# Kernel tuning notes

Hardware: AMD Instinct MI355X
Metric: run time of the kernel (lower is better)

## Reference

```python
import jax, jax.numpy as jnp
import numpy as np

N_MET = 250_000
N_RXN = 500_000
E_SUB = 2_000_000
E_ALL = 4_000_000
HIDDEN = 64
MSG_DIM = 32
DT = 0.01  # flux-limiting step size (forward called with dt > 0)


def setup_inputs() -> dict:
    key = jax.random.key(0)
    ks = jax.random.split(key, 12)
    inp = {}
    inp["x"] = jax.random.uniform(ks[0], (N_MET, 8), dtype=jnp.float32)
    inp["met_sub"] = jax.random.randint(ks[1], (E_SUB,), 0, N_MET, dtype=jnp.int32)
    inp["rxn_sub"] = jax.random.randint(ks[2], (E_SUB,), 0, N_RXN, dtype=jnp.int32)
    inp["sto_sub"] = jax.random.uniform(ks[3], (E_SUB,), dtype=jnp.float32) + 0.5  # |s_ij| > 0
    inp["met_all"] = jax.random.randint(ks[4], (E_ALL,), 0, N_MET, dtype=jnp.int32)
    inp["rxn_all"] = jax.random.randint(ks[5], (E_ALL,), 0, N_RXN, dtype=jnp.int32)
    inp["sto_all"] = jax.random.normal(ks[6], (E_ALL,), dtype=jnp.float32)
    sc = lambda fan_in: 1.0 / np.sqrt(fan_in)
    inp["W1"] = jax.random.normal(ks[7], (2, HIDDEN), dtype=jnp.float32) * sc(2)
    inp["b1"] = jnp.zeros((HIDDEN,), jnp.float32)
    inp["W2"] = jax.random.normal(ks[8], (HIDDEN, MSG_DIM), dtype=jnp.float32) * sc(HIDDEN)
    inp["b2"] = jnp.zeros((MSG_DIM,), jnp.float32)
    inp["W3"] = jax.random.normal(ks[9], (MSG_DIM, HIDDEN), dtype=jnp.float32) * sc(MSG_DIM)
    inp["b3"] = jnp.zeros((HIDDEN,), jnp.float32)
    inp["W4"] = jax.random.normal(ks[10], (HIDDEN, 1), dtype=jnp.float32) * sc(HIDDEN)
    inp["b4"] = jnp.zeros((1,), jnp.float32)
    inp["log_k"] = jax.random.uniform(ks[11], (N_RXN,), dtype=jnp.float32, minval=-3.0, maxval=-1.0)
    return inp


def reference(x, met_sub, rxn_sub, sto_sub, met_all, rxn_all, sto_all,
              W1, b1, W2, b2, W3, b3, W4, b4, log_k):
    conc = x[:, 3]                                            # [n_met]
    # per-substrate-edge message: MLP([conc_src, |s|]) -> msg_dim
    msg_in = jnp.stack([conc[met_sub], sto_sub], axis=-1)     # [E_sub, 2]
    msg = jnp.tanh(msg_in @ W1 + b1) @ W2 + b2                # [E_sub, msg_dim]
    # aggregate messages per reaction (index_add)
    h_rxn = jax.ops.segment_sum(msg, rxn_sub, num_segments=N_RXN)  # [n_rxn, msg_dim]
    # non-negative rates
    k = jnp.power(10.0, log_k)
    r = (jnp.tanh(h_rxn @ W3 + b3) @ W4 + b4)[:, 0]           # [n_rxn]
    v = k * jax.nn.softplus(r)
    # flux limiting: scale rates so no substrate is over-consumed in one dt step
    consumption = sto_sub * v[rxn_sub] * DT                   # [E_sub]
    total = jax.ops.segment_sum(consumption, met_sub, num_segments=N_MET)
    active = total > 1e-12
    met_scale = jnp.where(active,
                          jnp.minimum(conc / jnp.where(active, total, 1.0), 1.0),
                          1.0)                                # [n_met]
    edge_scale = met_scale[met_sub]
    rxn_scale = jnp.ones((N_RXN,), v.dtype).at[rxn_sub].min(edge_scale)  # amin, include_self
    v = v * rxn_scale
    # dx/dt = scatter-add of signed stoich * rate over all edges
    contrib = sto_all * v[rxn_all]                            # [E_all]
    dxdt = jax.ops.segment_sum(contrib, met_all, num_segments=N_MET)
    return dxdt[:, None]                                      # [n_met, 1]
```

## Files before the change

### kernel.cpp

```cpp
#include <hip/hip_runtime.h>

#define N_MET 250000
#define N_RXN 500000
#define N_RXN_PAD 500032
#define E_SUB 2000000
#define E_ALL 4000000
#define DT 0.01f

#define RXN_PER_BLK 256
#define THREADS 256
#define EDGE_CAP 1536

#define MV_RPB 64

#define BINSZ 1024
#define NBINS ((N_MET + BINSZ - 1) / BINSZ)
#define PART_EPB 4096
#define PART_NBLK ((E_ALL + PART_EPB - 1) / PART_EPB)
#define SPART_NBLK ((E_SUB + PART_EPB - 1) / PART_EPB)
#define RBINSZ 1024
#define RNBINS ((N_RXN + RBINSZ - 1) / RBINSZ)
#define RPART_NBLK ((E_SUB + PART_EPB - 1) / PART_EPB)
#define RBIN_CAP 6144

typedef int v4i __attribute__((ext_vector_type(4)));
typedef float v4f __attribute__((ext_vector_type(4)));
typedef short bf16x8 __attribute__((ext_vector_type(8)));
typedef float f32x4 __attribute__((ext_vector_type(4)));

static __device__ __forceinline__ float fast_tanh(float x) {
  float e = __expf(x + x);
  return 1.0f - __fdividef(2.0f, e + 1.0f);
}

static __device__ __forceinline__ int bcast_i(int v, int lane) {
  return __builtin_amdgcn_readlane(v, lane);
}

static __device__ __forceinline__ unsigned short bf16_rn(float f) {
  unsigned u = __float_as_uint(f);
  unsigned r = u + 0x7FFFu + ((u >> 16) & 1u);
  return (unsigned short)(r >> 16);
}

__global__ void k_pre(const float* __restrict__ W2, const float* __restrict__ W3,
                      const float* __restrict__ b2,
                      uint4* __restrict__ wfh, uint4* __restrict__ wfl,
                      float* __restrict__ b2w3) {
  int tid = blockIdx.x * blockDim.x + threadIdx.x;
  if (tid < 512) {
    int lane = tid & 63, jt = (tid >> 6) & 3, ks = tid >> 8;
    int jj = jt * 16 + (lane & 15);
    unsigned short h[8], l[8];
    #pragma unroll
    for (int t = 0; t < 8; ++t) {
      int kk = ks * 32 + (lane >> 4) * 8 + t;
      float w = 0.f;
      #pragma unroll
      for (int m = 0; m < 32; ++m) w = fmaf(W2[kk * 32 + m], W3[m * 64 + jj], w);
      h[t] = bf16_rn(w);
      float hf = __uint_as_float(((unsigned)h[t]) << 16);
      l[t] = bf16_rn(w - hf);
    }
    uint4 H, L;
    H.x = (unsigned)h[0] | ((unsigned)h[1] << 16);
    H.y = (unsigned)h[2] | ((unsigned)h[3] << 16);
    H.z = (unsigned)h[4] | ((unsigned)h[5] << 16);
    H.w = (unsigned)h[6] | ((unsigned)h[7] << 16);
    L.x = (unsigned)l[0] | ((unsigned)l[1] << 16);
    L.y = (unsigned)l[2] | ((unsigned)l[3] << 16);
    L.z = (unsigned)l[4] | ((unsigned)l[5] << 16);
    L.w = (unsigned)l[6] | ((unsigned)l[7] << 16);
    int idx = (ks * 4 + jt) * 64 + lane;
    wfh[idx] = H; wfl[idx] = L;
  }
  if (tid < 64) {
    float t = 0.f;
    #pragma unroll
    for (int m = 0; m < 32; ++m) t = fmaf(b2[m], W3[m * 64 + tid], t);
    b2w3[tid] = t;
  }
}

__global__ void k_conc(const float* __restrict__ x, float* __restrict__ conc) {
  int m = blockIdx.x * blockDim.x + threadIdx.x;
  if (m < N_MET) conc[m] = __builtin_nontemporal_load(x + m * 8 + 3);
}


template <int NB>
static __device__ __forceinline__ void bc_body(const int* __restrict__ keys, int nkeys,
                                               int* __restrict__ blk_cnt, int nblk) {
  __shared__ int cnt[NB];
  int b = blockIdx.x, t = threadIdx.x;
  for (int i = t; i < NB; i += 256) cnt[i] = 0;
  __syncthreads();
  int base = b * PART_EPB;
  #pragma unroll
  for (int i = 0; i < PART_EPB / 256; ++i) {
    int e = base + i * 256 + t;
    if (e < nkeys) atomicAdd(&cnt[__builtin_nontemporal_load(keys + e) >> 10], 1);
  }
  __syncthreads();
  for (int i = t; i < NB; i += 256) blk_cnt[i * nblk + b] = cnt[i];
}

__global__ __launch_bounds__(256) void k_bc_all(const int* __restrict__ met_all,
                                                int* __restrict__ blk_cnt) {
  bc_body<NBINS>(met_all, E_ALL, blk_cnt, PART_NBLK);
}
__global__ __launch_bounds__(256) void k_bc_sub(const int* __restrict__ met_sub,
                                                int* __restrict__ blk_cnt) {
  bc_body<NBINS>(met_sub, E_SUB, blk_cnt, SPART_NBLK);
}
__global__ __launch_bounds__(256) void k_rbc(const int* __restrict__ rxn_sub,
                                             int* __restrict__ blk_cnt) {
  bc_body<RNBINS>(rxn_sub, E_SUB, blk_cnt, RPART_NBLK);
}

__global__ __launch_bounds__(256) void k_bscan1(const int* __restrict__ blk_cnt,
                                                int* __restrict__ blk_pref,
                                                int* __restrict__ bin_tot, int nblk) {
  __shared__ int ss[256];
  int j = blockIdx.x, t = threadIdx.x;
  int carry = 0;
  for (int c = 0; c < nblk; c += 256) {
    int idx = c + t;
    int v = (idx < nblk) ? blk_cnt[j * nblk + idx] : 0;
    ss[t] = v; __syncthreads();
    for (int d = 1; d < 256; d <<= 1) {
      int a = (t >= d) ? ss[t - d] : 0;
      __syncthreads();
      ss[t] += a;
      __syncthreads();
    }
    if (idx < nblk) blk_pref[j * nblk + idx] = carry + ss[t] - v;
    carry += ss[255];
    __syncthreads();
  }
  if (t == 0) bin_tot[j] = carry;
}

__global__ __launch_bounds__(512) void k_bscan2(const int* __restrict__ bin_tot,
                                                int* __restrict__ bin_start, int n) {
  __shared__ int ss[512];
  int t = threadIdx.x;
  int v = (t < n) ? bin_tot[t] : 0;
  ss[t] = v; __syncthreads();
  for (int d = 1; d < 512; d <<= 1) {
    int a = (t >= d) ? ss[t - d] : 0;
    __syncthreads();
    ss[t] += a;
    __syncthreads();
  }
  if (t < n) bin_start[t] = ss[t] - v;
}

template <int NB, typename MakeRec>
static __device__ __forceinline__ void part_sorted(
    const int* __restrict__ keys, int nkeys, int nblk,
    const int* __restrict__ blk_pref, const int* __restrict__ bin_start,
    int2* __restrict__ out, MakeRec make) {
  __shared__ int2 ordered[PART_EPB];
  __shared__ unsigned short binb[PART_EPB];
  __shared__ int cnt[NB];
  __shared__ int gofs[NB];
  __shared__ int ss[256];
  int b = blockIdx.x, t = threadIdx.x;
  for (int i = t; i < NB; i += 256) cnt[i] = 0;
  __syncthreads();
  int base = b * PART_EPB;
  int kbuf[PART_EPB / 256];
  #pragma unroll
  for (int i = 0; i < PART_EPB / 256; ++i) {
    int e = base + i * 256 + t;
    kbuf[i] = (e < nkeys) ? __builtin_nontemporal_load(keys + e) : -1;
    if (kbuf[i] >= 0) atomicAdd(&cnt[kbuf[i] >> 10], 1);
  }
  __syncthreads();
  int nloc = 0;
  for (int c = 0; c < NB; c += 256) {
    int idx = c + t;
    int v = (idx < NB) ? cnt[idx] : 0;
    ss[t] = v; __syncthreads();
    for (int d = 1; d < 256; d <<= 1) {
      int a = (t >= d) ? ss[t - d] : 0;
      __syncthreads();
      ss[t] += a;
      __syncthreads();
    }
    int tot = ss[255];
    if (idx < NB) {
      int ls = nloc + ss[t] - v;
      cnt[idx] = ls;
      gofs[idx] = bin_start[idx] + blk_pref[idx * nblk + b] - ls;
    }
    nloc += tot;
    __syncthreads();
  }
  #pragma unroll
  for (int i = 0; i < PART_EPB / 256; ++i) {
    int k = kbuf[i];
    if (k >= 0) {
      int e = base + i * 256 + t;
      int bin = k >> 10;
      int2 rec = make(e, k);
      int pos = atomicAdd(&cnt[bin], 1);
      ordered[pos] = rec;
      binb[pos] = (unsigned short)bin;
    }
  }
  __syncthreads();
  for (int i = t; i < nloc; i += 256) {
    int2 rec = ordered[i];
    out[gofs[binb[i]] + i] = rec;
  }
}

__global__ __launch_bounds__(256) void k_rpart(
    const int* __restrict__ rxn_sub, const int* __restrict__ met_sub,
    const float* __restrict__ sto_sub,
    const int* __restrict__ blk_pref, const int* __restrict__ bin_start,
    int2* __restrict__ bins_rxn) {
  part_sorted<RNBINS>(rxn_sub, E_SUB, RPART_NBLK, blk_pref, bin_start, bins_rxn,
    [=] __device__ (int e, int k) {
      int m = __builtin_nontemporal_load(met_sub + e);
      float st = __builtin_nontemporal_load(sto_sub + e);
      int2 rec; rec.x = ((k & (RBINSZ - 1)) << 18) | m; rec.y = __float_as_int(st);
      return rec;
    });
}

__global__ __launch_bounds__(256) void k_part_sub(
    const int* __restrict__ met_sub, const int* __restrict__ rxn_sub,
    const float* __restrict__ sto_sub, const float* __restrict__ v_pre,
    const int* __restrict__ blk_pref, const int* __restrict__ bin_start,
    int2* __restrict__ bins_sub) {
  part_sorted<NBINS>(met_sub, E_SUB, SPART_NBLK, blk_pref, bin_start, bins_sub,
    [=] __device__ (int e, int k) {
      int r = __builtin_nontemporal_load(rxn_sub + e);
      float st = __builtin_nontemporal_load(sto_sub + e);
      float val = st * v_pre[r] * DT;
      int2 rec; rec.x = k & (BINSZ - 1); rec.y = __float_as_int(val);
      return rec;
    });
}

__global__ __launch_bounds__(256) void k_part(
    const int* __restrict__ met_all, const int* __restrict__ rxn_all,
    const float* __restrict__ sto_all, const float* __restrict__ vfin,
    const int* __restrict__ blk_pref, const int* __restrict__ bin_start,
    int2* __restrict__ bins) {
  part_sorted<NBINS>(met_all, E_ALL, PART_NBLK, blk_pref, bin_start, bins,
    [=] __device__ (int e, int k) {
      int r = __builtin_nontemporal_load(rxn_all + e);
      float st = __builtin_nontemporal_load(sto_all + e);
      float val = st * vfin[r];
      int2 rec; rec.x = k & (BINSZ - 1); rec.y = __float_as_int(val);
      return rec;
    });
}

__global__ __launch_bounds__(256) void k_rbin(
    const int2* __restrict__ bins_rxn, const int* __restrict__ rbin_start,
    const int* __restrict__ rbin_tot, int2* __restrict__ edges8, int* __restrict__ off) {
  __shared__ int2 stage[RBIN_CAP];
  __shared__ int lcnt[RBINSZ];
  __shared__ int lcur[RBINSZ];
  __shared__ int ss[256];
  int j = blockIdx.x, t = threadIdx.x;
  int base = rbin_start[j], n = rbin_tot[j];
  for (int i = t; i < RBINSZ; i += 256) lcnt[i] = 0;
  __syncthreads();
  bool fits = (n <= RBIN_CAP);
  if (fits) {
    for (int i = t; i < n; i += 256) {
      int2 rec = bins_rxn[base + i];
      stage[i] = rec;
      atomicAdd(&lcnt[((unsigned)rec.x) >> 18], 1);
    }
  } else {
    for (int i = t; i < n; i += 256) {
      int2 rec = bins_rxn[base + i];
      atomicAdd(&lcnt[((unsigned)rec.x) >> 18], 1);
    }
  }
  __syncthreads();
  int s0 = lcnt[4 * t], s1 = lcnt[4 * t + 1], s2 = lcnt[4 * t + 2], s3 = lcnt[4 * t + 3];
  int tsum = s0 + s1 + s2 + s3;
  ss[t] = tsum; __syncthreads();
  for (int d = 1; d < 256; d <<= 1) {
    int a = (t >= d) ? ss[t - d] : 0;
    __syncthreads();
    ss[t] += a;
    __syncthreads();
  }
  int run = ss[t] - tsum;
  lcur[4 * t] = run;
  lcur[4 * t + 1] = run + s0;
  lcur[4 * t + 2] = run + s0 + s1;
  lcur[4 * t + 3] = run + s0 + s1 + s2;
  __syncthreads();
  int R0 = j * RBINSZ;
  for (int rl = t; rl < RBINSZ; rl += 256) {
    int r = R0 + rl;
    if (r < N_RXN) off[r] = base + lcur[rl];
  }
  if (j == 0 && t == 0) off[N_RXN] = E_SUB;
  __syncthreads();
  if (fits) {
    for (int i = t; i < n; i += 256) {
      int2 rec = stage[i];
      int pos = atomicAdd(&lcur[((unsigned)rec.x) >> 18], 1);
      int2 out; out.x = rec.x & 0x3FFFF; out.y = rec.y;
      edges8[base + pos] = out;
    }
  } else {
    for (int i = t; i < n; i += 256) {
      int2 rec = bins_rxn[base + i];
      int pos = atomicAdd(&lcur[((unsigned)rec.x) >> 18], 1);
      int2 out; out.x = rec.x & 0x3FFFF; out.y = rec.y;
      edges8[base + pos] = out;
    }
  }
}

static __device__ __forceinline__ float edge_sum_lds(int o0, int o1, int estart,
                                                     const float2* ep,
                                                     float w1x, float w1y, float b1j) {
  float T0 = 0.f, T1 = 0.f;
  int c = o0;
  for (; c + 1 < o1; c += 2) {
    float2 e0 = ep[c - estart];
    float2 e1 = ep[c + 1 - estart];
    T0 += fast_tanh(fmaf(e0.x, w1x, fmaf(e0.y, w1y, b1j)));
    T1 += fast_tanh(fmaf(e1.x, w1x, fmaf(e1.y, w1y, b1j)));
  }
  if (c < o1) {
    float2 e0 = ep[c - estart];
    T0 += fast_tanh(fmaf(e0.x, w1x, fmaf(e0.y, w1y, b1j)));
  }
  return T0 + T1;
}

static __device__ __forceinline__ float edge_sum_glob(int o0, int o1,
                                                      const int2* edges8,
                                                      const float* conc,
                                                      float w1x, float w1y, float b1j) {
  float T = 0.f;
  for (int c = o0; c < o1; ++c) {
    int2 rec = edges8[c];
    float cc = conc[rec.x];
    T += fast_tanh(fmaf(cc, w1x, fmaf(__int_as_float(rec.y), w1y, b1j)));
  }
  return T;
}

__global__ __launch_bounds__(THREADS) void k_edge(
    const int* __restrict__ off, const int2* __restrict__ edges8,
    const float* __restrict__ conc,
    const float* __restrict__ W1, const float* __restrict__ b1,
    unsigned short* __restrict__ Thi, unsigned short* __restrict__ Tlo, int use_lo) {
  __shared__ int off_s[RXN_PER_BLK + 1];
  __shared__ float2 se[EDGE_CAP];

  int tid = threadIdx.x;
  int lane = tid & 63;
  int wv = tid >> 6;
  int R0 = blockIdx.x * RXN_PER_BLK;

  for (int i = tid; i <= RXN_PER_BLK; i += THREADS) {
    int r = R0 + i;
    off_s[i] = off[r > N_RXN ? N_RXN : r];
  }
  __syncthreads();
  int estart = off_s[0];
  int nE = off_s[RXN_PER_BLK] - estart;
  bool fits = (nE <= EDGE_CAP);
  if (fits) {
    for (int i = tid; i < nE; i += THREADS) {
      int2 rec = edges8[estart + i];
      se[i] = make_float2(conc[rec.x], __int_as_float(rec.y));
    }
  }

  float w1x = W1[lane], w1y = W1[64 + lane], b1j = b1[lane];

  int rbase = R0 + wv * 64;
  int o0l = off_s[wv * 64 + lane];
  int o1l = off_s[wv * 64 + lane + 1];

  __syncthreads();

  #pragma clang loop unroll(disable)
  for (int i = 0; i < 64; ++i) {
    int r = rbase + i;
    if (r >= N_RXN) break;
    int o0 = bcast_i(o0l, i), o1 = bcast_i(o1l, i);
    float T = fits ? edge_sum_lds(o0, o1, estart, se, w1x, w1y, b1j)
                   : edge_sum_glob(o0, o1, edges8, conc, w1x, w1y, b1j);
    unsigned short hi = bf16_rn(T);
    Thi[r * 64 + lane] = hi;
    if (use_lo) {
      float hf = __uint_as_float(((unsigned)hi) << 16);
      Tlo[r * 64 + lane] = bf16_rn(T - hf);
    }
  }
}

__global__ __launch_bounds__(256) void k_mv(
    const int* __restrict__ off,
    const unsigned short* __restrict__ Thi, const unsigned short* __restrict__ Tlo,
    const uint4* __restrict__ wfh, const uint4* __restrict__ wfl,
    const float* __restrict__ b2w3, const float* __restrict__ b3,
    const float* __restrict__ W4, const float* __restrict__ b4,
    const float* __restrict__ log_k, int use_lo, float* __restrict__ v_pre) {
  __shared__ int soff[MV_RPB + 1];
  int tid = threadIdx.x, lane = tid & 63, w = tid >> 6;
  int B0 = blockIdx.x * MV_RPB;
  for (int i = tid; i <= MV_RPB; i += 256) {
    int r = B0 + i;
    soff[i] = off[r > N_RXN ? N_RXN : r];
  }
  __syncthreads();

  int R0 = B0 + w * 16;
  int col = lane & 15, rowg = lane >> 4;

  bf16x8 ah[2], al[2];
  {
    int rowelem = (R0 + col) * 64 + rowg * 8;
    const uint4* ph = (const uint4*)Thi;
    ah[0] = __builtin_bit_cast(bf16x8, ph[rowelem >> 3]);
    ah[1] = __builtin_bit_cast(bf16x8, ph[(rowelem + 32) >> 3]);
    if (use_lo) {
      const uint4* pl = (const uint4*)Tlo;
      al[0] = __builtin_bit_cast(bf16x8, pl[rowelem >> 3]);
      al[1] = __builtin_bit_cast(bf16x8, pl[(rowelem + 32) >> 3]);
    }
  }

  f32x4 acc[4];
  #pragma unroll
  for (int jt = 0; jt < 4; ++jt) acc[jt] = (f32x4){0.f, 0.f, 0.f, 0.f};

  #pragma unroll
  for (int jt = 0; jt < 4; ++jt) {
    #pragma unroll
    for (int ks = 0; ks < 2; ++ks) {
      int bidx = (ks * 4 + jt) * 64 + lane;
      bf16x8 bh = __builtin_bit_cast(bf16x8, wfh[bidx]);
      acc[jt] = __builtin_amdgcn_mfma_f32_16x16x32_bf16(ah[ks], bh, acc[jt], 0, 0, 0);
      if (use_lo) {
        bf16x8 bl = __builtin_bit_cast(bf16x8, wfl[bidx]);
        acc[jt] = __builtin_amdgcn_mfma_f32_16x16x32_bf16(ah[ks], bl, acc[jt], 0, 0, 0);
        acc[jt] = __builtin_amdgcn_mfma_f32_16x16x32_bf16(al[ks], bh, acc[jt], 0, 0, 0);
      }
    }
  }

  float w4c[4], bwc[4], b3c[4];
  #pragma unroll
  for (int jt = 0; jt < 4; ++jt) {
    int jj = jt * 16 + col;
    w4c[jt] = W4[jj]; bwc[jt] = b2w3[jj]; b3c[jt] = b3[jj];
  }
  float b40 = b4[0];

  float nq[4];
  #pragma unroll
  for (int q = 0; q < 4; ++q) {
    int idx = w * 16 + rowg * 4 + q;
    nq[q] = (float)(soff[idx + 1] - soff[idx]);
  }

  #pragma unroll
  for (int q = 0; q < 4; ++q) {
    float s = 0.f;
    #pragma unroll
    for (int jt = 0; jt < 4; ++jt) {
      float u = acc[jt][q] + nq[q] * bwc[jt] + b3c[jt];
      s += fast_tanh(u) * w4c[jt];
    }
    s += __shfl_xor(s, 1, 64);
    s += __shfl_xor(s, 2, 64);
    s += __shfl_xor(s, 4, 64);
    s += __shfl_xor(s, 8, 64);
    if (col == 0) {
      int r = R0 + rowg * 4 + q;
      float lk = (r < N_RXN) ? log_k[r] : 0.f;
      float racc = s + b40;
      float k10 = __expf(lk * 2.3025850929940457f);
      float sp = (racc > 15.f) ? racc : __logf(1.f + __expf(racc));
      if (r < N_RXN) v_pre[r] = k10 * sp;
    }
  }
}

__global__ __launch_bounds__(256) void k_bins_sub(
    const int2* __restrict__ bins_sub, const int* __restrict__ bin_start,
    const int* __restrict__ bin_tot, const float* __restrict__ conc,
    float* __restrict__ met_scale) {
  __shared__ float acc[BINSZ];
  int j = blockIdx.x, t = threadIdx.x;
  for (int i = t; i < BINSZ; i += 256) acc[i] = 0.f;
  __syncthreads();
  int s0 = bin_start[j], n = bin_tot[j];
  for (int i = t; i < n; i += 256) {
    int2 rec = bins_sub[s0 + i];
    atomicAdd(&acc[rec.x], __int_as_float(rec.y));
  }
  __syncthreads();
  int m0 = j * BINSZ;
  for (int i = t; i < BINSZ; i += 256) {
    int m = m0 + i;
    if (m < N_MET) {
      float tot = acc[i];
      met_scale[m] = (tot > 1e-12f) ? fminf(conc[m] / tot, 1.0f) : 1.0f;
    }
  }
}

__global__ __launch_bounds__(256) void k_rscale(
    const int* __restrict__ off, const int2* __restrict__ edges8,
    const float* __restrict__ met_scale, const float* __restrict__ v_pre,
    float* __restrict__ vfin) {
  __shared__ int soff[MV_RPB + 1];
  int tid = threadIdx.x, lane = tid & 63, w = tid >> 6;
  int B0 = blockIdx.x * MV_RPB;
  for (int i = tid; i <= MV_RPB; i += 256) {
    int r = B0 + i;
    soff[i] = off[r > N_RXN ? N_RXN : r];
  }
  __syncthreads();

  int rloc = w * 16 + (lane >> 2);
  int o0 = soff[rloc], o1 = soff[rloc + 1];
  float sc = 1.0f;
  for (int c = o0 + (lane & 3); c < o1; c += 4) {
    sc = fminf(sc, met_scale[edges8[c].x]);
  }
  sc = fminf(sc, __shfl_xor(sc, 1, 64));
  sc = fminf(sc, __shfl_xor(sc, 2, 64));
  if ((lane & 3) == 0) {
    int r = B0 + rloc;
    if (r < N_RXN) vfin[r] = v_pre[r] * sc;
  }
}

__global__ __launch_bounds__(256) void k_bins(const int2* __restrict__ bins,
                                              const int* __restrict__ bin_start,
                                              const int* __restrict__ bin_tot,
                                              float* __restrict__ dxdt) {
  __shared__ float acc[BINSZ];
  int j = blockIdx.x, t = threadIdx.x;
  for (int i = t; i < BINSZ; i += 256) acc[i] = 0.f;
  __syncthreads();
  int s0 = bin_start[j], n = bin_tot[j];
  for (int i = t; i < n; i += 256) {
    int2 rec = bins[s0 + i];
    atomicAdd(&acc[rec.x], __int_as_float(rec.y));
  }
  __syncthreads();
  int m0 = j * BINSZ;
  for (int i = t; i < BINSZ; i += 256) {
    int m = m0 + i;
    if (m < N_MET) dxdt[m] = acc[i];
  }
}

extern "C" void kernel_launch(void* const* d_in, const int* in_sizes, int n_in,
                              void* d_out, int out_size, void* d_ws, size_t ws_size,
                              hipStream_t stream) {
  const float* x       = (const float*)d_in[0];
  const int*   met_sub = (const int*)d_in[1];
  const int*   rxn_sub = (const int*)d_in[2];
  const float* sto_sub = (const float*)d_in[3];
  const int*   met_all = (const int*)d_in[4];
  const int*   rxn_all = (const int*)d_in[5];
  const float* sto_all = (const float*)d_in[6];
  const float* W1    = (const float*)d_in[7];
  const float* b1    = (const float*)d_in[8];
  const float* W2    = (const float*)d_in[9];
  const float* b2    = (const float*)d_in[10];
  const float* W3    = (const float*)d_in[11];
  const float* b3    = (const float*)d_in[12];
  const float* W4    = (const float*)d_in[13];
  const float* b4    = (const float*)d_in[14];
  const float* log_k = (const float*)d_in[15];
  float* dxdt = (float*)d_out;

  char* ws = (char*)d_ws;
  size_t p = 0;
  auto alloc = [&](size_t bytes) -> void* {
    void* r = (void*)(ws + p);
    p += (bytes + 255) & ~(size_t)255;
    return r;
  };
  int*    off        = (int*)alloc(sizeof(int) * (N_RXN + 1));
  uint4*  wfh        = (uint4*)alloc(sizeof(uint4) * 512);
  uint4*  wfl        = (uint4*)alloc(sizeof(uint4) * 512);
  float*  b2w3       = (float*)alloc(sizeof(float) * 64);
  float*  v_pre      = (float*)alloc(sizeof(float) * N_RXN);
  float*  vfin       = (float*)alloc(sizeof(float) * N_RXN);
  float*  conc       = (float*)alloc(sizeof(float) * N_MET);
  float*  met_scale  = (float*)alloc(sizeof(float) * N_MET);
  int2*   edges8     = (int2*)alloc(sizeof(int2) * E_SUB);
  int2*   bins_rxn   = (int2*)alloc(sizeof(int2) * E_SUB);
  int2*   bins_sub   = (int2*)alloc(sizeof(int2) * E_SUB);
  int2*   bins       = (int2*)alloc(sizeof(int2) * E_ALL);
  int*    rblk_cnt   = (int*)alloc(sizeof(int) * RNBINS * RPART_NBLK);
  int*    rblk_pref  = (int*)alloc(sizeof(int) * RNBINS * RPART_NBLK);
  int*    sblk_cnt   = (int*)alloc(sizeof(int) * NBINS * SPART_NBLK);
  int*    sblk_pref  = (int*)alloc(sizeof(int) * NBINS * SPART_NBLK);
  int*    blk_cnt    = (int*)alloc(sizeof(int) * NBINS * PART_NBLK);
  int*    blk_pref   = (int*)alloc(sizeof(int) * NBINS * PART_NBLK);
  int*    rbin_tot   = (int*)alloc(sizeof(int) * 512);
  int*    rbin_start = (int*)alloc(sizeof(int) * 512);
  int*    sbin_tot   = (int*)alloc(sizeof(int) * 512);
  int*    sbin_start = (int*)alloc(sizeof(int) * 512);
  int*    bin_tot    = (int*)alloc(sizeof(int) * 512);
  int*    bin_start  = (int*)alloc(sizeof(int) * 512);
  unsigned short* Thi = (unsigned short*)alloc(sizeof(unsigned short) * (size_t)N_RXN_PAD * 64);
  size_t tlo_bytes = sizeof(unsigned short) * (size_t)N_RXN_PAD * 64;
  int use_lo = (p + tlo_bytes <= ws_size) ? 1 : 0;
  unsigned short* Tlo = use_lo ? (unsigned short*)alloc(tlo_bytes) : Thi;
  (void)in_sizes; (void)n_in; (void)out_size;


  k_pre<<<2, 256, 0, stream>>>(W2, W3, b2, wfh, wfl, b2w3);
  k_conc<<<(N_MET + 255) / 256, 256, 0, stream>>>(x, conc);

  k_rbc<<<RPART_NBLK, 256, 0, stream>>>(rxn_sub, rblk_cnt);
  k_bc_sub<<<SPART_NBLK, 256, 0, stream>>>(met_sub, sblk_cnt);
  k_bc_all<<<PART_NBLK, 256, 0, stream>>>(met_all, blk_cnt);
  k_bscan1<<<RNBINS, 256, 0, stream>>>(rblk_cnt, rblk_pref, rbin_tot, RPART_NBLK);
  k_bscan1<<<NBINS, 256, 0, stream>>>(sblk_cnt, sblk_pref, sbin_tot, SPART_NBLK);
  k_bscan1<<<NBINS, 256, 0, stream>>>(blk_cnt, blk_pref, bin_tot, PART_NBLK);
  k_bscan2<<<1, 512, 0, stream>>>(rbin_tot, rbin_start, RNBINS);
  k_bscan2<<<1, 512, 0, stream>>>(sbin_tot, sbin_start, NBINS);
  k_bscan2<<<1, 512, 0, stream>>>(bin_tot, bin_start, NBINS);

  k_rpart<<<RPART_NBLK, 256, 0, stream>>>(rxn_sub, met_sub, sto_sub,
                                          rblk_pref, rbin_start, bins_rxn);
  k_rbin<<<RNBINS, 256, 0, stream>>>(bins_rxn, rbin_start, rbin_tot, edges8, off);

  k_edge<<<(N_RXN + RXN_PER_BLK - 1) / RXN_PER_BLK, THREADS, 0, stream>>>(
      off, edges8, conc, W1, b1, Thi, Tlo, use_lo);
  k_mv<<<(N_RXN + MV_RPB - 1) / MV_RPB, 256, 0, stream>>>(
      off, Thi, Tlo, wfh, wfl, b2w3, b3, W4, b4, log_k, use_lo, v_pre);

  k_part_sub<<<SPART_NBLK, 256, 0, stream>>>(met_sub, rxn_sub, sto_sub, v_pre,
                                             sblk_pref, sbin_start, bins_sub);
  k_bins_sub<<<NBINS, 256, 0, stream>>>(bins_sub, sbin_start, sbin_tot, conc, met_scale);

  k_rscale<<<(N_RXN + MV_RPB - 1) / MV_RPB, 256, 0, stream>>>(
      off, edges8, met_scale, v_pre, vfin);

  k_part<<<PART_NBLK, 256, 0, stream>>>(met_all, rxn_all, sto_all, vfin,
                                        blk_pref, bin_start, bins);
  k_bins<<<NBINS, 256, 0, stream>>>(bins, bin_start, bin_tot, dxdt);
}
```

Before: 516.7 us.

## Merge preprocessing launches and simplify per-edge tanh accumulation

Eleven small setup launches (weight precompute, conc extraction, three bin-count passes, and three pairs of scans) become three kernels that pick their role from the block index, cutting launch overhead and serial gaps. The per-edge tanh sum is rewritten as count minus twice a sum of 1/(exp2(k*t)+1), with the 2*log2(e) constant folded into W1 and b1, so each edge costs one exp2 and one reciprocal. The loop also carries o0 forward instead of reading it per reaction. This trades slight numerical differences from the hardware rcp/exp2 approximations for fewer instructions per edge.

```diff
diff --git a/kernel.cpp b/kernel.cpp
--- a/kernel.cpp
+++ b/kernel.cpp
@@ -28,6 +28,17 @@
 typedef short bf16x8 __attribute__((ext_vector_type(8)));
 typedef float f32x4 __attribute__((ext_vector_type(4)));
 
+#if __has_builtin(__builtin_amdgcn_exp2f)
+#define EXP2F(x) __builtin_amdgcn_exp2f(x)
+#else
+#define EXP2F(x) exp2f(x)
+#endif
+#if __has_builtin(__builtin_amdgcn_rcpf)
+#define RCPF(x) __builtin_amdgcn_rcpf(x)
+#else
+#define RCPF(x) __fdividef(1.0f, (x))
+#endif
+
 static __device__ __forceinline__ float fast_tanh(float x) {
   float e = __expf(x + x);
   return 1.0f - __fdividef(2.0f, e + 1.0f);
@@ -43,86 +54,79 @@
   return (unsigned short)(r >> 16);
 }
 
-__global__ void k_pre(const float* __restrict__ W2, const float* __restrict__ W3,
-                      const float* __restrict__ b2,
-                      uint4* __restrict__ wfh, uint4* __restrict__ wfl,
-                      float* __restrict__ b2w3) {
-  int tid = blockIdx.x * blockDim.x + threadIdx.x;
-  if (tid < 512) {
-    int lane = tid & 63, jt = (tid >> 6) & 3, ks = tid >> 8;
-    int jj = jt * 16 + (lane & 15);
-    unsigned short h[8], l[8];
-    #pragma unroll
-    for (int t = 0; t < 8; ++t) {
-      int kk = ks * 32 + (lane >> 4) * 8 + t;
-      float w = 0.f;
-      #pragma unroll
-      for (int m = 0; m < 32; ++m) w = fmaf(W2[kk * 32 + m], W3[m * 64 + jj], w);
-      h[t] = bf16_rn(w);
-      float hf = __uint_as_float(((unsigned)h[t]) << 16);
-      l[t] = bf16_rn(w - hf);
-    }
-    uint4 H, L;
-    H.x = (unsigned)h[0] | ((unsigned)h[1] << 16);
-    H.y = (unsigned)h[2] | ((unsigned)h[3] << 16);
-    H.z = (unsigned)h[4] | ((unsigned)h[5] << 16);
-    H.w = (unsigned)h[6] | ((unsigned)h[7] << 16);
-    L.x = (unsigned)l[0] | ((unsigned)l[1] << 16);
-    L.y = (unsigned)l[2] | ((unsigned)l[3] << 16);
-    L.z = (unsigned)l[4] | ((unsigned)l[5] << 16);
-    L.w = (unsigned)l[6] | ((unsigned)l[7] << 16);
-    int idx = (ks * 4 + jt) * 64 + lane;
-    wfh[idx] = H; wfl[idx] = L;
-  }
-  if (tid < 64) {
-    float t = 0.f;
-    #pragma unroll
-    for (int m = 0; m < 32; ++m) t = fmaf(b2[m], W3[m * 64 + tid], t);
-    b2w3[tid] = t;
-  }
-}
-
-__global__ void k_conc(const float* __restrict__ x, float* __restrict__ conc) {
-  int m = blockIdx.x * blockDim.x + threadIdx.x;
-  if (m < N_MET) conc[m] = __builtin_nontemporal_load(x + m * 8 + 3);
-}
-
-
-template <int NB>
-static __device__ __forceinline__ void bc_body(const int* __restrict__ keys, int nkeys,
-                                               int* __restrict__ blk_cnt, int nblk) {
-  __shared__ int cnt[NB];
+__global__ __launch_bounds__(256) void k_bc3(
+    const int* __restrict__ rxn_sub, const int* __restrict__ met_sub,
+    const int* __restrict__ met_all,
+    const float* __restrict__ x, float* __restrict__ conc,
+    const float* __restrict__ W2, const float* __restrict__ W3,
+    const float* __restrict__ b2,
+    uint4* __restrict__ wfh, uint4* __restrict__ wfl, float* __restrict__ b2w3,
+    int* __restrict__ rblk_cnt, int* __restrict__ sblk_cnt, int* __restrict__ blk_cnt) {
+  __shared__ int cnt[RNBINS];
   int b = blockIdx.x, t = threadIdx.x;
-  for (int i = t; i < NB; i += 256) cnt[i] = 0;
-  __syncthreads();
-  int base = b * PART_EPB;
+  const int* keys; int nkeys, nblk, nb, bl; int* out;
+  if (b < RPART_NBLK) {
+    keys = rxn_sub; nkeys = E_SUB; nblk = RPART_NBLK; nb = RNBINS; out = rblk_cnt; bl = b;
+    if (b < 2) {
+      int tid = b * 256 + t;
+      if (tid < 512) {
+        int lane = tid & 63, jt = (tid >> 6) & 3, ks = tid >> 8;
+        int jj = jt * 16 + (lane & 15);
+        unsigned short h[8], l[8];
+        #pragma unroll
+        for (int q = 0; q < 8; ++q) {
+          int kk = ks * 32 + (lane >> 4) * 8 + q;
+          float w = 0.f;
+          #pragma unroll
+          for (int m = 0; m < 32; ++m) w = fmaf(W2[kk * 32 + m], W3[m * 64 + jj], w);
+          h[q] = bf16_rn(w);
+          float hf = __uint_as_float(((unsigned)h[q]) << 16);
+          l[q] = bf16_rn(w - hf);
+        }
+        uint4 H, L;
+        H.x = (unsigned)h[0] | ((unsigned)h[1] << 16);
+        H.y = (unsigned)h[2] | ((unsigned)h[3] << 16);
+        H.z = (unsigned)h[4] | ((unsigned)h[5] << 16);
+        H.w = (unsigned)h[6] | ((unsigned)h[7] << 16);
+        L.x = (unsigned)l[0] | ((unsigned)l[1] << 16);
+        L.y = (unsigned)l[2] | ((unsigned)l[3] << 16);
+        L.z = (unsigned)l[4] | ((unsigned)l[5] << 16);
+        L.w = (unsigned)l[6] | ((unsigned)l[7] << 16);
+        int idx = (ks * 4 + jt) * 64 + lane;
+        wfh[idx] = H; wfl[idx] = L;
+      }
+      if (tid < 64) {
+        float s = 0.f;
+        #pragma unroll
+        for (int m = 0; m < 32; ++m) s = fmaf(b2[m], W3[m * 64 + tid], s);
+        b2w3[tid] = s;
+      }
+    }
+  } else if (b < RPART_NBLK + SPART_NBLK) {
+    keys = met_sub; nkeys = E_SUB; nblk = SPART_NBLK; nb = NBINS; out = sblk_cnt;
+    bl = b - RPART_NBLK;
+  } else {
+    keys = met_all; nkeys = E_ALL; nblk = PART_NBLK; nb = NBINS; out = blk_cnt;
+    bl = b - RPART_NBLK - SPART_NBLK;
+    int m = bl * 256 + t;
+    if (m < N_MET) conc[m] = __builtin_nontemporal_load(x + m * 8 + 3);
+  }
+  for (int i = t; i < nb; i += 256) cnt[i] = 0;
+  __syncthreads();
+  int base = bl * PART_EPB;
   #pragma unroll
   for (int i = 0; i < PART_EPB / 256; ++i) {
     int e = base + i * 256 + t;
     if (e < nkeys) atomicAdd(&cnt[__builtin_nontemporal_load(keys + e) >> 10], 1);
   }
   __syncthreads();
-  for (int i = t; i < NB; i += 256) blk_cnt[i * nblk + b] = cnt[i];
-}
-
-__global__ __launch_bounds__(256) void k_bc_all(const int* __restrict__ met_all,
-                                                int* __restrict__ blk_cnt) {
-  bc_body<NBINS>(met_all, E_ALL, blk_cnt, PART_NBLK);
-}
-__global__ __launch_bounds__(256) void k_bc_sub(const int* __restrict__ met_sub,
-                                                int* __restrict__ blk_cnt) {
-  bc_body<NBINS>(met_sub, E_SUB, blk_cnt, SPART_NBLK);
-}
-__global__ __launch_bounds__(256) void k_rbc(const int* __restrict__ rxn_sub,
-                                             int* __restrict__ blk_cnt) {
-  bc_body<RNBINS>(rxn_sub, E_SUB, blk_cnt, RPART_NBLK);
-}
-
-__global__ __launch_bounds__(256) void k_bscan1(const int* __restrict__ blk_cnt,
-                                                int* __restrict__ blk_pref,
-                                                int* __restrict__ bin_tot, int nblk) {
-  __shared__ int ss[256];
-  int j = blockIdx.x, t = threadIdx.x;
+  for (int i = t; i < nb; i += 256) out[i * nblk + bl] = cnt[i];
+}
+
+static __device__ __forceinline__ void scan1_body(int* ss,
+    const int* __restrict__ blk_cnt, int* __restrict__ blk_pref,
+    int* __restrict__ bin_tot, int nblk, int j) {
+  int t = threadIdx.x;
   int carry = 0;
   for (int c = 0; c < nblk; c += 256) {
     int idx = c + t;
@@ -141,11 +145,31 @@
   if (t == 0) bin_tot[j] = carry;
 }
 
-__global__ __launch_bounds__(512) void k_bscan2(const int* __restrict__ bin_tot,
-                                                int* __restrict__ bin_start, int n) {
+__global__ __launch_bounds__(256) void k_scan1all(
+    const int* __restrict__ rblk_cnt, int* __restrict__ rblk_pref, int* __restrict__ rbin_tot,
+    const int* __restrict__ sblk_cnt, int* __restrict__ sblk_pref, int* __restrict__ sbin_tot,
+    const int* __restrict__ blk_cnt, int* __restrict__ blk_pref, int* __restrict__ bin_tot) {
+  __shared__ int ss[256];
+  int b = blockIdx.x;
+  if (b < RNBINS)
+    scan1_body(ss, rblk_cnt, rblk_pref, rbin_tot, RPART_NBLK, b);
+  else if (b < RNBINS + NBINS)
+    scan1_body(ss, sblk_cnt, sblk_pref, sbin_tot, SPART_NBLK, b - RNBINS);
+  else
+    scan1_body(ss, blk_cnt, blk_pref, bin_tot, PART_NBLK, b - RNBINS - NBINS);
+}
+
+__global__ __launch_bounds__(512) void k_scan2all(
+    const int* __restrict__ rbin_tot, int* __restrict__ rbin_start,
+    const int* __restrict__ sbin_tot, int* __restrict__ sbin_start,
+    const int* __restrict__ bin_tot, int* __restrict__ bin_start) {
   __shared__ int ss[512];
+  const int* tot; int* st; int n;
+  if (blockIdx.x == 0)      { tot = rbin_tot; st = rbin_start; n = RNBINS; }
+  else if (blockIdx.x == 1) { tot = sbin_tot; st = sbin_start; n = NBINS; }
+  else                      { tot = bin_tot;  st = bin_start;  n = NBINS; }
   int t = threadIdx.x;
-  int v = (t < n) ? bin_tot[t] : 0;
+  int v = (t < n) ? tot[t] : 0;
   ss[t] = v; __syncthreads();
   for (int d = 1; d < 512; d <<= 1) {
     int a = (t >= d) ? ss[t - d] : 0;
@@ -153,7 +177,7 @@
     ss[t] += a;
     __syncthreads();
   }
-  if (t < n) bin_start[t] = ss[t] - v;
+  if (t < n) st[t] = ss[t] - v;
 }
 
 template <int NB, typename MakeRec>
@@ -325,35 +349,39 @@
   }
 }
 
-static __device__ __forceinline__ float edge_sum_lds(int o0, int o1, int estart,
-                                                     const float2* ep,
-                                                     float w1x, float w1y, float b1j) {
-  float T0 = 0.f, T1 = 0.f;
+static __device__ __forceinline__ float edge_rsum_lds(int o0, int o1, int estart,
+                                                      const float2* ep,
+                                                      float w1x, float w1y, float b1j) {
+  float S0 = 0.f, S1 = 0.f;
   int c = o0;
   for (; c + 1 < o1; c += 2) {
     float2 e0 = ep[c - estart];
     float2 e1 = ep[c + 1 - estart];
-    T0 += fast_tanh(fmaf(e0.x, w1x, fmaf(e0.y, w1y, b1j)));
-    T1 += fast_tanh(fmaf(e1.x, w1x, fmaf(e1.y, w1y, b1j)));
+    float t0 = fmaf(e0.x, w1x, fmaf(e0.y, w1y, b1j));
+    float t1 = fmaf(e1.x, w1x, fmaf(e1.y, w1y, b1j));
+    S0 += RCPF(EXP2F(t0) + 1.0f);
+    S1 += RCPF(EXP2F(t1) + 1.0f);
   }
   if (c < o1) {
     float2 e0 = ep[c - estart];
-    T0 += fast_tanh(fmaf(e0.x, w1x, fmaf(e0.y, w1y, b1j)));
-  }
-  return T0 + T1;
-}
-
-static __device__ __forceinline__ float edge_sum_glob(int o0, int o1,
-                                                      const int2* edges8,
-                                                      const float* conc,
-                                                      float w1x, float w1y, float b1j) {
-  float T = 0.f;
+    float t0 = fmaf(e0.x, w1x, fmaf(e0.y, w1y, b1j));
+    S0 += RCPF(EXP2F(t0) + 1.0f);
+  }
+  return S0 + S1;
+}
+
+static __device__ __forceinline__ float edge_rsum_glob(int o0, int o1,
+                                                       const int2* edges8,
+                                                       const float* conc,
+                                                       float w1x, float w1y, float b1j) {
+  float S = 0.f;
   for (int c = o0; c < o1; ++c) {
     int2 rec = edges8[c];
     float cc = conc[rec.x];
-    T += fast_tanh(fmaf(cc, w1x, fmaf(__int_as_float(rec.y), w1y, b1j)));
-  }
-  return T;
+    float t0 = fmaf(cc, w1x, fmaf(__int_as_float(rec.y), w1y, b1j));
+    S += RCPF(EXP2F(t0) + 1.0f);
+  }
+  return S;
 }
 
 __global__ __launch_bounds__(THREADS) void k_edge(
@@ -384,7 +412,8 @@
     }
   }
 
-  float w1x = W1[lane], w1y = W1[64 + lane], b1j = b1[lane];
+  const float C2 = 2.8853900817779268f;
+  float w1x = W1[lane] * C2, w1y = W1[64 + lane] * C2, b1j = b1[lane] * C2;
 
   int rbase = R0 + wv * 64;
   int o0l = off_s[wv * 64 + lane];
@@ -392,19 +421,22 @@
 
   __syncthreads();
 
+  int o0 = bcast_i(o0l, 0);
   #pragma clang loop unroll(disable)
   for (int i = 0; i < 64; ++i) {
     int r = rbase + i;
     if (r >= N_RXN) break;
-    int o0 = bcast_i(o0l, i), o1 = bcast_i(o1l, i);
-    float T = fits ? edge_sum_lds(o0, o1, estart, se, w1x, w1y, b1j)
-                   : edge_sum_glob(o0, o1, edges8, conc, w1x, w1y, b1j);
+    int o1 = bcast_i(o1l, i);
+    float S = fits ? edge_rsum_lds(o0, o1, estart, se, w1x, w1y, b1j)
+                   : edge_rsum_glob(o0, o1, edges8, conc, w1x, w1y, b1j);
+    float T = (float)(o1 - o0) - 2.0f * S;
     unsigned short hi = bf16_rn(T);
     Thi[r * 64 + lane] = hi;
     if (use_lo) {
       float hf = __uint_as_float(((unsigned)hi) << 16);
       Tlo[r * 64 + lane] = bf16_rn(T - hf);
     }
+    o0 = o1;
   }
 }
 
@@ -628,18 +660,14 @@
   (void)in_sizes; (void)n_in; (void)out_size;
 
 
-  k_pre<<<2, 256, 0, stream>>>(W2, W3, b2, wfh, wfl, b2w3);
-  k_conc<<<(N_MET + 255) / 256, 256, 0, stream>>>(x, conc);
-
-  k_rbc<<<RPART_NBLK, 256, 0, stream>>>(rxn_sub, rblk_cnt);
-  k_bc_sub<<<SPART_NBLK, 256, 0, stream>>>(met_sub, sblk_cnt);
-  k_bc_all<<<PART_NBLK, 256, 0, stream>>>(met_all, blk_cnt);
-  k_bscan1<<<RNBINS, 256, 0, stream>>>(rblk_cnt, rblk_pref, rbin_tot, RPART_NBLK);
-  k_bscan1<<<NBINS, 256, 0, stream>>>(sblk_cnt, sblk_pref, sbin_tot, SPART_NBLK);
-  k_bscan1<<<NBINS, 256, 0, stream>>>(blk_cnt, blk_pref, bin_tot, PART_NBLK);
-  k_bscan2<<<1, 512, 0, stream>>>(rbin_tot, rbin_start, RNBINS);
-  k_bscan2<<<1, 512, 0, stream>>>(sbin_tot, sbin_start, NBINS);
-  k_bscan2<<<1, 512, 0, stream>>>(bin_tot, bin_start, NBINS);
+  k_bc3<<<RPART_NBLK + SPART_NBLK + PART_NBLK, 256, 0, stream>>>(
+      rxn_sub, met_sub, met_all, x, conc, W2, W3, b2, wfh, wfl, b2w3,
+      rblk_cnt, sblk_cnt, blk_cnt);
+  k_scan1all<<<RNBINS + NBINS + NBINS, 256, 0, stream>>>(
+      rblk_cnt, rblk_pref, rbin_tot, sblk_cnt, sblk_pref, sbin_tot,
+      blk_cnt, blk_pref, bin_tot);
+  k_scan2all<<<3, 512, 0, stream>>>(rbin_tot, rbin_start, sbin_tot, sbin_start,
+                                    bin_tot, bin_start);
 
   k_rpart<<<RPART_NBLK, 256, 0, stream>>>(rxn_sub, met_sub, sto_sub,
                                           rblk_pref, rbin_start, bins_rxn);
```

Result: faster. 458.1 us (-11.3%).
